# Performance work log

Hardware: AMD Instinct MI355X
Metric: run time of the kernel (lower is better)

Reference implementation:

```python
import jax, jax.numpy as jnp
import numpy as np

H = 4          # heads (hardcoded in original forward via shp=(4, ...))
B, G, D = 2, 2048, 128
KD = VD = 32   # key_dim = val_dim = embed_dim // n_heads
E = 128        # embed_dim


def setup_inputs() -> dict:
    key = jax.random.key(0)
    ks = jax.random.split(key, 10)
    s = lambda d: 1.0 / np.sqrt(d)
    return {
        "h": jax.random.normal(ks[0], (B, G, D), jnp.float32),
        "out_source_attn": jax.random.normal(ks[1], (H, B, G, G), jnp.float32),
        "Wq": jax.random.uniform(ks[2], (H, D, KD), jnp.float32, -s(KD), s(KD)),
        "Wk": jax.random.uniform(ks[3], (H, D, KD), jnp.float32, -s(KD), s(KD)),
        "Wv": jax.random.uniform(ks[4], (H, D, VD), jnp.float32, -s(VD), s(VD)),
        "Wout": jax.random.uniform(ks[5], (H, KD, E), jnp.float32, -s(E), s(E)),
        "w1": jax.random.uniform(ks[6], (8, 8), jnp.float32, -s(8), s(8)),
        "b1": jax.random.uniform(ks[7], (8,), jnp.float32, -s(8), s(8)),
        "w2": jax.random.uniform(ks[8], (4, 8), jnp.float32, -s(8), s(8)),
        "b2": jax.random.uniform(ks[9], (4,), jnp.float32, -s(4), s(4)),
    }


def reference(h, out_source_attn, Wq, Wk, Wv, Wout, w1, b1, w2, b2):
    # Per-head projections: (H, B, G, kd/vd)
    Q = jnp.einsum('bgd,hdk->hbgk', h, Wq)
    K = jnp.einsum('bgd,hdk->hbgk', h, Wk)
    V = jnp.einsum('bgd,hdv->hbgv', h, Wv)
    # QK^T scores concat with external attention source: (2H=8, B, G, G)
    scores = jnp.einsum('hbqk,hbpk->hbqp', Q, K)
    compat = jnp.concatenate([scores, out_source_attn], axis=0)
    # Per-score small MLP (Linear(8,8)->ReLU->Linear(8,4)) over channel dim
    x = compat.transpose(1, 2, 3, 0)                 # (B, G, G, 8)
    x = jax.nn.relu(x @ w1.T + b1) @ w2.T + b2       # (B, G, G, 4)
    attn = jax.nn.softmax(x.transpose(3, 0, 1, 2), axis=-1)  # (H, B, G, G)
    heads = jnp.einsum('hbqp,hbpv->hbqv', attn, V)   # (H, B, G, VD)
    out = jnp.einsum('hbqv,hve->bqe', heads, Wout)   # (B, G, E)
    return (out, out_source_attn)
```

## Files before the change

kernel.cpp:

```cpp
#include <hip/hip_runtime.h>

typedef __attribute__((ext_vector_type(8))) short bf16x8;
typedef __attribute__((ext_vector_type(4))) float f32x4;

#define OUT0 524288
#define SRC_CH_STRIDE 8388608
#define PART_HEAD 544
#define PART_SLICE 2176

__device__ __forceinline__ unsigned short f2bf(float x){
    unsigned u = __builtin_bit_cast(unsigned, x);
    u += 0x7FFFu + ((u >> 16) & 1u);
    return (unsigned short)(u >> 16);
}

__global__ __launch_bounds__(256) void qkv_kernel(
    const float* __restrict__ hsrc,
    const float* __restrict__ Wq, const float* __restrict__ Wk, const float* __restrict__ Wv,
    unsigned short* __restrict__ Qb, unsigned short* __restrict__ Kb, unsigned short* __restrict__ Vt)
{
    __shared__ float hs[32*128];
    __shared__ float ws[128*32];
    const int t = threadIdx.x;
    const int g0 = blockIdx.x * 32;
    const int mat = blockIdx.y;
    const int mt = mat >> 2, head = mat & 3;
    {
        const float4* s = (const float4*)(hsrc + g0*128);
        float4* d = (float4*)hs;
        #pragma unroll
        for (int i=0;i<4;i++) d[t + i*256] = s[t + i*256];
        const float* W = (mt==0?Wq:(mt==1?Wk:Wv)) + head*4096;
        const float4* s2 = (const float4*)W;
        float4* d2 = (float4*)ws;
        #pragma unroll
        for (int i=0;i<4;i++) d2[t + i*256] = s2[t + i*256];
    }
    __syncthreads();
    const int r = t >> 3;
    const int k0 = (t & 7) * 4;
    float a0=0.f,a1=0.f,a2=0.f,a3=0.f;
    const float* hr = hs + r*128;
    #pragma unroll 8
    for (int d=0; d<128; d++){
        float hv = hr[d];
        float4 w4 = *(const float4*)(ws + d*32 + k0);
        a0 = fmaf(hv, w4.x, a0); a1 = fmaf(hv, w4.y, a1);
        a2 = fmaf(hv, w4.z, a2); a3 = fmaf(hv, w4.w, a3);
    }
    const int row_g = g0 + r;
    if (mt == 2){
        const int b = row_g >> 11, g = row_g & 2047;
        unsigned short* dst = Vt + ((b*128 + head*32 + k0) * 2048) + g;
        dst[0] = f2bf(a0); dst[2048] = f2bf(a1); dst[4096] = f2bf(a2); dst[6144] = f2bf(a3);
    } else {
        unsigned short* dst = (mt==0?Qb:Kb) + row_g*128 + head*32 + k0;
        dst[0]=f2bf(a0); dst[1]=f2bf(a1); dst[2]=f2bf(a2); dst[3]=f2bf(a3);
    }
}

__global__ __launch_bounds__(256) void attn_kernel(
    const float* __restrict__ src,
    const unsigned short* __restrict__ Qb,
    const unsigned short* __restrict__ Kb,
    const unsigned short* __restrict__ Vt,
    const float* __restrict__ w1g, const float* __restrict__ b1g,
    const float* __restrict__ w2g, const float* __restrict__ b2g,
    float* __restrict__ part,
    float* __restrict__ out)
{
    __shared__ __align__(16) float S_lds[4*16*68];
    __shared__ __align__(16) unsigned short Pb_lds[4*16*72];
    __shared__ __align__(16) float wt[112];
    __shared__ __align__(16) float m_lds[64];
    __shared__ __align__(16) float l_lds[64];
    __shared__ __align__(16) float alpha_lds[64];

    const int t = threadIdx.x;
    const int lane = t & 63;
    const int c = t >> 6;
    const int quad = lane >> 4;
    const int lrow = lane & 15;
    const int q0 = blockIdx.x * 16;
    const int b = blockIdx.y;
    const int s = blockIdx.z;
    const int pbase = s * 512;

    if (t < 64) wt[t] = w1g[t];
    else if (t < 72) wt[t] = b1g[t-64];
    else if (t < 104) wt[t] = w2g[t-72];
    else if (t < 108) wt[t] = b2g[t-104];
    if (t < 64){ m_lds[t] = -1e30f; l_lds[t] = 0.f; alpha_lds[t] = 0.f; }

    const bf16x8 qf = *(const bf16x8*)(Qb + (b*2048 + q0 + lrow)*128 + c*32 + quad*8);

    const int mq = t >> 4;
    const int mp = (t & 15) * 4;
    const int srcbase0 = (b*2048 + q0 + mq)*2048 + mp;

    f32x4 o0 = {0.f,0.f,0.f,0.f};
    f32x4 o1 = {0.f,0.f,0.f,0.f};
    const f32x4 zero4 = {0.f,0.f,0.f,0.f};

    __syncthreads();

    for (int p0 = pbase; p0 < pbase + 512; p0 += 64){
        float4 r4[4];
        #pragma unroll
        for (int ch=0; ch<4; ch++)
            r4[ch] = *(const float4*)(src + srcbase0 + ch*SRC_CH_STRIDE + p0);
        #pragma unroll
        for (int sub=0; sub<4; sub++){
            const bf16x8 kf = *(const bf16x8*)(Kb + (b*2048 + p0 + sub*16 + lrow)*128 + c*32 + quad*8);
            f32x4 sacc = __builtin_amdgcn_mfma_f32_16x16x32_bf16(qf, kf, zero4, 0, 0, 0);
            float* Sp = S_lds + (c*16 + quad*4)*68 + sub*16 + lrow;
            Sp[0] = sacc[0]; Sp[68] = sacc[1]; Sp[136] = sacc[2]; Sp[204] = sacc[3];
        }
        #pragma unroll
        for (int ch=0; ch<4; ch++)
            *(float4*)(out + OUT0 + srcbase0 + ch*SRC_CH_STRIDE + p0) = r4[ch];
        __syncthreads();

        {
            float xs[4][4], xr[4][4];
            #pragma unroll
            for (int ch=0; ch<4; ch++){
                float4 v = *(const float4*)(S_lds + (ch*16 + mq)*68 + mp);
                xs[ch][0]=v.x; xs[ch][1]=v.y; xs[ch][2]=v.z; xs[ch][3]=v.w;
                xr[ch][0]=r4[ch].x; xr[ch][1]=r4[ch].y; xr[ch][2]=r4[ch].z; xr[ch][3]=r4[ch].w;
            }
            float z[4][4];
            #pragma unroll
            for (int cc=0; cc<4; cc++){
                float bb = wt[104+cc];
                #pragma unroll
                for (int cell=0; cell<4; cell++) z[cc][cell] = bb;
            }
            #pragma unroll
            for (int j=0; j<8; j++){
                float w0 = wt[j*8+0], w1v = wt[j*8+1], w2v = wt[j*8+2], w3 = wt[j*8+3];
                float w4v = wt[j*8+4], w5 = wt[j*8+5], w6 = wt[j*8+6], w7 = wt[j*8+7];
                float bj = wt[64+j];
                float hcell[4];
                #pragma unroll
                for (int cell=0; cell<4; cell++){
                    float v = bj;
                    v = fmaf(w0, xs[0][cell], v);
                    v = fmaf(w1v, xs[1][cell], v);
                    v = fmaf(w2v, xs[2][cell], v);
                    v = fmaf(w3, xs[3][cell], v);
                    v = fmaf(w4v, xr[0][cell], v);
                    v = fmaf(w5, xr[1][cell], v);
                    v = fmaf(w6, xr[2][cell], v);
                    v = fmaf(w7, xr[3][cell], v);
                    hcell[cell] = fmaxf(v, 0.f);
                }
                #pragma unroll
                for (int cc=0; cc<4; cc++){
                    float wv = wt[72 + cc*8 + j];
                    #pragma unroll
                    for (int cell=0; cell<4; cell++) z[cc][cell] = fmaf(wv, hcell[cell], z[cc][cell]);
                }
            }
            #pragma unroll
            for (int ch=0; ch<4; ch++){
                float4 v; v.x=z[ch][0]; v.y=z[ch][1]; v.z=z[ch][2]; v.w=z[ch][3];
                *(float4*)(S_lds + (ch*16 + mq)*68 + mp) = v;
            }
        }
        __syncthreads();

        {
            const int rowid = t >> 2;
            const int seg = t & 3;
            const float* Sp = S_lds + rowid*68 + seg*16;
            float4 xa = *(const float4*)(Sp);
            float4 xb = *(const float4*)(Sp+4);
            float4 xc = *(const float4*)(Sp+8);
            float4 xd = *(const float4*)(Sp+12);
            float x[16];
            x[0]=xa.x; x[1]=xa.y; x[2]=xa.z; x[3]=xa.w;
            x[4]=xb.x; x[5]=xb.y; x[6]=xb.z; x[7]=xb.w;
            x[8]=xc.x; x[9]=xc.y; x[10]=xc.z; x[11]=xc.w;
            x[12]=xd.x; x[13]=xd.y; x[14]=xd.z; x[15]=xd.w;
            float mloc = x[0];
            #pragma unroll
            for (int i=1;i<16;i++) mloc = fmaxf(mloc, x[i]);
            mloc = fmaxf(mloc, __shfl_xor(mloc, 1));
            mloc = fmaxf(mloc, __shfl_xor(mloc, 2));
            float m_old = m_lds[rowid];
            float m_new = fmaxf(m_old, mloc);
            float ssum = 0.f;
            unsigned pk[8];
            #pragma unroll
            for (int i=0;i<8;i++){
                float e0 = __expf(x[2*i] - m_new);
                float e1 = __expf(x[2*i+1] - m_new);
                ssum += e0 + e1;
                pk[i] = (unsigned)f2bf(e0) | ((unsigned)f2bf(e1) << 16);
            }
            ssum += __shfl_xor(ssum, 1);
            ssum += __shfl_xor(ssum, 2);
            uint4* Pp = (uint4*)(Pb_lds + rowid*72 + seg*16);
            Pp[0] = make_uint4(pk[0],pk[1],pk[2],pk[3]);
            Pp[1] = make_uint4(pk[4],pk[5],pk[6],pk[7]);
            if (seg == 0){
                float alpha = __expf(m_old - m_new);
                m_lds[rowid] = m_new;
                alpha_lds[rowid] = alpha;
                l_lds[rowid] = fmaf(l_lds[rowid], alpha, ssum);
            }
        }
        __syncthreads();

        {
            float4 a4 = *(const float4*)(alpha_lds + c*16 + quad*4);
            o0[0]*=a4.x; o0[1]*=a4.y; o0[2]*=a4.z; o0[3]*=a4.w;
            o1[0]*=a4.x; o1[1]*=a4.y; o1[2]*=a4.z; o1[3]*=a4.w;
            #pragma unroll
            for (int chunk=0; chunk<2; chunk++){
                const bf16x8 pf = *(const bf16x8*)(Pb_lds + (c*16 + lrow)*72 + chunk*32 + quad*8);
                const bf16x8 v0 = *(const bf16x8*)(Vt + (b*128 + c*32 + lrow)*2048 + p0 + chunk*32 + quad*8);
                const bf16x8 v1 = *(const bf16x8*)(Vt + (b*128 + c*32 + 16 + lrow)*2048 + p0 + chunk*32 + quad*8);
                o0 = __builtin_amdgcn_mfma_f32_16x16x32_bf16(pf, v0, o0, 0, 0, 0);
                o1 = __builtin_amdgcn_mfma_f32_16x16x32_bf16(pf, v1, o1, 0, 0, 0);
            }
        }
    }

    {
        float* P = part + (((b*128 + blockIdx.x)*4 + s)*4 + c) * PART_HEAD;
        if (lane < 16){
            P[lane]      = m_lds[c*16 + lane];
            P[16 + lane] = l_lds[c*16 + lane];
        }
        #pragma unroll
        for (int r=0;r<4;r++){
            P[32 + (quad*4 + r)*32 + lrow]      = o0[r];
            P[32 + (quad*4 + r)*32 + 16 + lrow] = o1[r];
        }
    }
}

__global__ __launch_bounds__(256) void combine_kernel(
    const float* __restrict__ part,
    const float* __restrict__ Wout,
    float* __restrict__ out)
{
    __shared__ __align__(16) float O_lds[64*33];
    const int t = threadIdx.x;
    const int qt = blockIdx.x, b = blockIdx.y;

    if (t < 64){
        const int c = t >> 4, q = t & 15;
        const float* P0 = part + (((b*128 + qt)*4 + 0)*4 + c) * PART_HEAD;
        float m0 = P0[q], m1 = P0[PART_SLICE + q], m2 = P0[2*PART_SLICE + q], m3 = P0[3*PART_SLICE + q];
        float M = fmaxf(fmaxf(m0, m1), fmaxf(m2, m3));
        float w0 = __expf(m0 - M), w1 = __expf(m1 - M), w2 = __expf(m2 - M), w3 = __expf(m3 - M);
        float L = P0[16+q]*w0 + P0[PART_SLICE+16+q]*w1 + P0[2*PART_SLICE+16+q]*w2 + P0[3*PART_SLICE+16+q]*w3;
        float invL = 1.f / L;
        const float* O0 = P0 + 32 + q*32;
        float* dst = O_lds + t*33;
        #pragma unroll
        for (int v4 = 0; v4 < 8; v4++){
            float4 a  = *(const float4*)(O0 + v4*4);
            float4 bb = *(const float4*)(O0 + PART_SLICE + v4*4);
            float4 cc = *(const float4*)(O0 + 2*PART_SLICE + v4*4);
            float4 dd = *(const float4*)(O0 + 3*PART_SLICE + v4*4);
            dst[v4*4+0] = (a.x*w0 + bb.x*w1 + cc.x*w2 + dd.x*w3) * invL;
            dst[v4*4+1] = (a.y*w0 + bb.y*w1 + cc.y*w2 + dd.y*w3) * invL;
            dst[v4*4+2] = (a.z*w0 + bb.z*w1 + cc.z*w2 + dd.z*w3) * invL;
            dst[v4*4+3] = (a.w*w0 + bb.w*w1 + cc.w*w2 + dd.w*w3) * invL;
        }
    }
    __syncthreads();

    {
        const int mq = t >> 4;
        const int e0 = (t & 15) * 8;
        float acc[8];
        #pragma unroll
        for (int i=0;i<8;i++) acc[i]=0.f;
        #pragma unroll
        for (int cc=0; cc<4; cc++){
            const float* OhRow = O_lds + (cc*16 + mq)*33;
            const float* Wrow = Wout + cc*32*128 + e0;
            #pragma unroll 4
            for (int v=0; v<32; v++){
                float ov = OhRow[v];
                float4 wA = *(const float4*)(Wrow + v*128);
                float4 wB = *(const float4*)(Wrow + v*128 + 4);
                acc[0]=fmaf(ov,wA.x,acc[0]); acc[1]=fmaf(ov,wA.y,acc[1]);
                acc[2]=fmaf(ov,wA.z,acc[2]); acc[3]=fmaf(ov,wA.w,acc[3]);
                acc[4]=fmaf(ov,wB.x,acc[4]); acc[5]=fmaf(ov,wB.y,acc[5]);
                acc[6]=fmaf(ov,wB.z,acc[6]); acc[7]=fmaf(ov,wB.w,acc[7]);
            }
        }
        float* op = out + (b*2048 + qt*16 + mq)*128 + e0;
        float4 oA; oA.x=acc[0]; oA.y=acc[1]; oA.z=acc[2]; oA.w=acc[3];
        float4 oB; oB.x=acc[4]; oB.y=acc[5]; oB.z=acc[6]; oB.w=acc[7];
        *(float4*)op = oA;
        *(float4*)(op+4) = oB;
    }
}

extern "C" void kernel_launch(void* const* d_in, const int* in_sizes, int n_in,
                              void* d_out, int out_size, void* d_ws, size_t ws_size,
                              hipStream_t stream) {
    const float* h    = (const float*)d_in[0];
    const float* src  = (const float*)d_in[1];
    const float* Wq   = (const float*)d_in[2];
    const float* Wk   = (const float*)d_in[3];
    const float* Wv   = (const float*)d_in[4];
    const float* Wout = (const float*)d_in[5];
    const float* w1   = (const float*)d_in[6];
    const float* b1   = (const float*)d_in[7];
    const float* w2   = (const float*)d_in[8];
    const float* b2   = (const float*)d_in[9];
    float* out = (float*)d_out;

    unsigned short* Qb = (unsigned short*)d_ws;
    unsigned short* Kb = Qb + 524288;
    unsigned short* Vt = Kb + 524288;
    float* part = (float*)((char*)d_ws + 3*1048576);

    qkv_kernel<<<dim3(128,12), 256, 0, stream>>>(h, Wq, Wk, Wv, Qb, Kb, Vt);
    attn_kernel<<<dim3(128,2,4), 256, 0, stream>>>(src, Qb, Kb, Vt, w1, b1, w2, b2, part, out);
    combine_kernel<<<dim3(128,2), 256, 0, stream>>>(part, Wout, out);
}
```

Measured before the change: 323.9 us.

## Double the split-K slices, prefetch source tiles and drop a barrier

The key dimension is split into 8 slices of 256 instead of 4 slices of 512, which doubles the number of attention blocks; the combine kernel is generalised to merge 8 partials. Inside the loop, the next source-attention tile is loaded into a second register buffer (double buffering), and V fragments are loaded early. One of the two block-wide barriers per iteration is removed. The aim is to hide global-load latency and raise occupancy, at the cost of more partial-result traffic, higher register use, and a possible LDS race on S_lds between iterations now that the barrier is gone.

```diff
diff --git a/kernel.cpp b/kernel.cpp
--- a/kernel.cpp
+++ b/kernel.cpp
@@ -7,6 +7,7 @@
 #define SRC_CH_STRIDE 8388608
 #define PART_HEAD 544
 #define PART_SLICE 2176
+#define NSLICE 8
 
 __device__ __forceinline__ unsigned short f2bf(float x){
     unsigned u = __builtin_bit_cast(unsigned, x);
@@ -84,7 +85,7 @@
     const int q0 = blockIdx.x * 16;
     const int b = blockIdx.y;
     const int s = blockIdx.z;
-    const int pbase = s * 512;
+    const int pbase = s * 256;
 
     if (t < 64) wt[t] = w1g[t];
     else if (t < 72) wt[t] = b1g[t-64];
@@ -102,13 +103,19 @@
     f32x4 o1 = {0.f,0.f,0.f,0.f};
     const f32x4 zero4 = {0.f,0.f,0.f,0.f};
 
+    float4 r4[2][4];
+    #pragma unroll
+    for (int ch=0; ch<4; ch++)
+        r4[0][ch] = *(const float4*)(src + srcbase0 + ch*SRC_CH_STRIDE + pbase);
+
     __syncthreads();
 
-    for (int p0 = pbase; p0 < pbase + 512; p0 += 64){
-        float4 r4[4];
-        #pragma unroll
-        for (int ch=0; ch<4; ch++)
-            r4[ch] = *(const float4*)(src + srcbase0 + ch*SRC_CH_STRIDE + p0);
+    #pragma unroll
+    for (int it = 0; it < 4; ++it){
+        const int p0 = pbase + it*64;
+        const int cur = it & 1;
+        const int nxt = cur ^ 1;
+
         #pragma unroll
         for (int sub=0; sub<4; sub++){
             const bf16x8 kf = *(const bf16x8*)(Kb + (b*2048 + p0 + sub*16 + lrow)*128 + c*32 + quad*8);
@@ -116,10 +123,21 @@
             float* Sp = S_lds + (c*16 + quad*4)*68 + sub*16 + lrow;
             Sp[0] = sacc[0]; Sp[68] = sacc[1]; Sp[136] = sacc[2]; Sp[204] = sacc[3];
         }
+        __syncthreads();
+
+        if (it < 3){
+            #pragma unroll
+            for (int ch=0; ch<4; ch++)
+                r4[nxt][ch] = *(const float4*)(src + srcbase0 + ch*SRC_CH_STRIDE + p0 + 64);
+        }
+        const unsigned short* Vrow = Vt + (b*128 + c*32 + lrow)*2048 + p0 + quad*8;
+        const bf16x8 vp0a = *(const bf16x8*)(Vrow);
+        const bf16x8 vp0b = *(const bf16x8*)(Vrow + 16*2048);
+        const bf16x8 vp1a = *(const bf16x8*)(Vrow + 32);
+        const bf16x8 vp1b = *(const bf16x8*)(Vrow + 16*2048 + 32);
         #pragma unroll
         for (int ch=0; ch<4; ch++)
-            *(float4*)(out + OUT0 + srcbase0 + ch*SRC_CH_STRIDE + p0) = r4[ch];
-        __syncthreads();
+            *(float4*)(out + OUT0 + srcbase0 + ch*SRC_CH_STRIDE + p0) = r4[cur][ch];
 
         {
             float xs[4][4], xr[4][4];
@@ -127,7 +145,7 @@
             for (int ch=0; ch<4; ch++){
                 float4 v = *(const float4*)(S_lds + (ch*16 + mq)*68 + mp);
                 xs[ch][0]=v.x; xs[ch][1]=v.y; xs[ch][2]=v.z; xs[ch][3]=v.w;
-                xr[ch][0]=r4[ch].x; xr[ch][1]=r4[ch].y; xr[ch][2]=r4[ch].z; xr[ch][3]=r4[ch].w;
+                xr[ch][0]=r4[cur][ch].x; xr[ch][1]=r4[cur][ch].y; xr[ch][2]=r4[cur][ch].z; xr[ch][3]=r4[cur][ch].w;
             }
             float z[4][4];
             #pragma unroll
@@ -211,25 +229,22 @@
                 l_lds[rowid] = fmaf(l_lds[rowid], alpha, ssum);
             }
         }
-        __syncthreads();
 
         {
             float4 a4 = *(const float4*)(alpha_lds + c*16 + quad*4);
             o0[0]*=a4.x; o0[1]*=a4.y; o0[2]*=a4.z; o0[3]*=a4.w;
             o1[0]*=a4.x; o1[1]*=a4.y; o1[2]*=a4.z; o1[3]*=a4.w;
-            #pragma unroll
-            for (int chunk=0; chunk<2; chunk++){
-                const bf16x8 pf = *(const bf16x8*)(Pb_lds + (c*16 + lrow)*72 + chunk*32 + quad*8);
-                const bf16x8 v0 = *(const bf16x8*)(Vt + (b*128 + c*32 + lrow)*2048 + p0 + chunk*32 + quad*8);
-                const bf16x8 v1 = *(const bf16x8*)(Vt + (b*128 + c*32 + 16 + lrow)*2048 + p0 + chunk*32 + quad*8);
-                o0 = __builtin_amdgcn_mfma_f32_16x16x32_bf16(pf, v0, o0, 0, 0, 0);
-                o1 = __builtin_amdgcn_mfma_f32_16x16x32_bf16(pf, v1, o1, 0, 0, 0);
-            }
+            const bf16x8 pf0 = *(const bf16x8*)(Pb_lds + (c*16 + lrow)*72 + quad*8);
+            const bf16x8 pf1 = *(const bf16x8*)(Pb_lds + (c*16 + lrow)*72 + 32 + quad*8);
+            o0 = __builtin_amdgcn_mfma_f32_16x16x32_bf16(pf0, vp0a, o0, 0, 0, 0);
+            o1 = __builtin_amdgcn_mfma_f32_16x16x32_bf16(pf0, vp0b, o1, 0, 0, 0);
+            o0 = __builtin_amdgcn_mfma_f32_16x16x32_bf16(pf1, vp1a, o0, 0, 0, 0);
+            o1 = __builtin_amdgcn_mfma_f32_16x16x32_bf16(pf1, vp1b, o1, 0, 0, 0);
         }
     }
 
     {
-        float* P = part + (((b*128 + blockIdx.x)*4 + s)*4 + c) * PART_HEAD;
+        float* P = part + (((b*128 + blockIdx.x)*NSLICE + s)*4 + c) * PART_HEAD;
         if (lane < 16){
             P[lane]      = m_lds[c*16 + lane];
             P[16 + lane] = l_lds[c*16 + lane];
@@ -253,24 +268,38 @@
 
     if (t < 64){
         const int c = t >> 4, q = t & 15;
-        const float* P0 = part + (((b*128 + qt)*4 + 0)*4 + c) * PART_HEAD;
-        float m0 = P0[q], m1 = P0[PART_SLICE + q], m2 = P0[2*PART_SLICE + q], m3 = P0[3*PART_SLICE + q];
-        float M = fmaxf(fmaxf(m0, m1), fmaxf(m2, m3));
-        float w0 = __expf(m0 - M), w1 = __expf(m1 - M), w2 = __expf(m2 - M), w3 = __expf(m3 - M);
-        float L = P0[16+q]*w0 + P0[PART_SLICE+16+q]*w1 + P0[2*PART_SLICE+16+q]*w2 + P0[3*PART_SLICE+16+q]*w3;
+        const float* P0 = part + (((b*128 + qt)*NSLICE + 0)*4 + c) * PART_HEAD;
+        float m[NSLICE];
+        #pragma unroll
+        for (int j=0;j<NSLICE;j++) m[j] = P0[j*PART_SLICE + q];
+        float M = m[0];
+        #pragma unroll
+        for (int j=1;j<NSLICE;j++) M = fmaxf(M, m[j]);
+        float w[NSLICE];
+        float L = 0.f;
+        #pragma unroll
+        for (int j=0;j<NSLICE;j++){
+            w[j] = __expf(m[j] - M);
+            L = fmaf(P0[j*PART_SLICE + 16 + q], w[j], L);
+        }
         float invL = 1.f / L;
         const float* O0 = P0 + 32 + q*32;
         float* dst = O_lds + t*33;
         #pragma unroll
         for (int v4 = 0; v4 < 8; v4++){
-            float4 a  = *(const float4*)(O0 + v4*4);
-            float4 bb = *(const float4*)(O0 + PART_SLICE + v4*4);
-            float4 cc = *(const float4*)(O0 + 2*PART_SLICE + v4*4);
-            float4 dd = *(const float4*)(O0 + 3*PART_SLICE + v4*4);
-            dst[v4*4+0] = (a.x*w0 + bb.x*w1 + cc.x*w2 + dd.x*w3) * invL;
-            dst[v4*4+1] = (a.y*w0 + bb.y*w1 + cc.y*w2 + dd.y*w3) * invL;
-            dst[v4*4+2] = (a.z*w0 + bb.z*w1 + cc.z*w2 + dd.z*w3) * invL;
-            dst[v4*4+3] = (a.w*w0 + bb.w*w1 + cc.w*w2 + dd.w*w3) * invL;
+            float ax=0.f, ay=0.f, az=0.f, aw=0.f;
+            #pragma unroll
+            for (int j=0;j<NSLICE;j++){
+                float4 a = *(const float4*)(O0 + j*PART_SLICE + v4*4);
+                ax = fmaf(a.x, w[j], ax);
+                ay = fmaf(a.y, w[j], ay);
+                az = fmaf(a.z, w[j], az);
+                aw = fmaf(a.w, w[j], aw);
+            }
+            dst[v4*4+0] = ax * invL;
+            dst[v4*4+1] = ay * invL;
+            dst[v4*4+2] = az * invL;
+            dst[v4*4+3] = aw * invL;
         }
     }
     __syncthreads();
@@ -325,6 +354,6 @@
     float* part = (float*)((char*)d_ws + 3*1048576);
 
     qkv_kernel<<<dim3(128,12), 256, 0, stream>>>(h, Wq, Wk, Wv, Qb, Kb, Vt);
-    attn_kernel<<<dim3(128,2,4), 256, 0, stream>>>(src, Qb, Kb, Vt, w1, b1, w2, b2, part, out);
+    attn_kernel<<<dim3(128,2,NSLICE), 256, 0, stream>>>(src, Qb, Kb, Vt, w1, b1, w2, b2, part, out);
     combine_kernel<<<dim3(128,2), 256, 0, stream>>>(part, Wout, out);
 }
```

New measurement: 327.5 us. No clear change (+1.1%).
